# Kernel tuning notes

Hardware: AMD Instinct MI355X
Metric: run time of the kernel (lower is better)

Reference implementation:

```python
import jax, jax.numpy as jnp
import numpy as np

RADIUS = 0.5
BATCH, N, C_IN, C_OUT = 8, 1024, 64, 64


def setup_inputs() -> dict:
    key = jax.random.key(0)
    k1, k2, k3 = jax.random.split(key, 3)
    features = jax.random.normal(k1, (BATCH, N, C_IN), dtype=jnp.float32)
    geometry = jax.random.normal(k2, (BATCH, N, 3), dtype=jnp.float32)
    # Kernel stand-in: linear map from relative position to [C_out, C_in] matrix
    W = jax.random.normal(k3, (3, C_OUT, C_IN), dtype=jnp.float32) / np.sqrt(3.0 * C_IN)
    return {"features": features, "geometry": geometry, "W": W}


def reference(features, geometry, W):
    # diff[z,a,b,:] = r_b - r_a  (neighbor minus center), matching rb - ra in torch
    diff = geometry[:, None, :, :] - geometry[:, :, None, :]          # [z,a,b,3]
    norm = jnp.sqrt(jnp.sum(diff * diff, axis=-1))                    # [z,a,b]
    # rel_mask: 1 where within radius (the dense equivalent of the padded
    # neighbor-list + mask; padded/out-of-ball entries contribute zero)
    rel_mask = (norm < RADIUS).astype(features.dtype)                 # [z,a,b]
    # kernel(diff)[z,a,b,i,j] = sum_x diff[z,a,b,x] * W[x,i,j]
    # output[z,a,i] = sum_{b,x,j} mask*diff[z,a,b,x] * W[x,i,j] * feat[z,b,j]
    mdiff = rel_mask[..., None] * diff                                # [z,a,b,3]
    tmp = jnp.einsum('zabx,zbj->zaxj', mdiff, features)               # [z,a,3,Cin]
    out = jnp.einsum('zaxj,xij->zai', tmp, W)                         # [z,a,Cout]
    return out
```

## Files before the change

### kernel.cpp

```cpp
#include <hip/hip_runtime.h>


#define BATCHSZ 8
#define NPTS 1024
#define CIN 64
#define COUT 64
#define NXJ (3 * CIN)
#define NG (NXJ / 4)
#define PPB 8
#define BS (PPB * 64)
#define CAP 128
#define GPW (NG / PPB)

#define SM_LR 3072
#define SM_TMP 7168
#define SM_TOTAL 8704

__global__ __launch_bounds__(256) void transpose_W_kernel(
    const float* __restrict__ W,
    float* __restrict__ Wt)
{
    const int t = blockIdx.x * 256 + threadIdx.x;
    if (t >= 3 * COUT * CIN) return;
    const int x = t >> 12;
    const int i = (t >> 6) & 63;
    const int j = t & 63;
    const int xj = x * CIN + j;
    Wt[((xj >> 2) * COUT + i) * 4 + (xj & 3)] = W[t];
}

template <bool WT>
__global__ __launch_bounds__(BS, 8) void neigh_conv_kernel(
    const float* __restrict__ feat,
    const float* __restrict__ geom,
    const float* __restrict__ Wv,
    float* __restrict__ out)
{
    const int lane = threadIdx.x & 63;
    const int wv   = threadIdx.x >> 6;
    const int p    = blockIdx.x * PPB + wv;
    const int a    = p & (NPTS - 1);
    const int z    = p >> 10;

    __shared__ __align__(16) float smem[SM_TOTAL];

    {
        const float4* src = (const float4*)(geom + (size_t)z * NPTS * 3);
        float4* dst = (float4*)smem;
        for (int k = threadIdx.x; k < NPTS * 3 / 4; k += BS)
            dst[k] = src[k];
    }
    __syncthreads();

    const float* geo = smem;
    const float gax = geo[a * 3 + 0];
    const float gay = geo[a * 3 + 1];
    const float gaz = geo[a * 3 + 2];
    const float* fz = feat + (size_t)z * NPTS * CIN;

    int*   lb = (int*)(smem + SM_LR) + wv * 512;
    float* lx = smem + SM_LR + wv * 512 + 128;
    float* ly = lx + 128;
    float* lz = ly + 128;

    const unsigned long long ltmask = (1ull << lane) - 1ull;
    float acc0 = 0.f, acc1 = 0.f, acc2 = 0.f;
    int nn = 0;

    #pragma unroll 4
    for (int bb = 0; bb < NPTS; bb += 64) {
        const int b = bb + lane;
        float dx, dy, dz, d2;
        {
            #pragma clang fp contract(off)
            dx = geo[b * 3 + 0] - gax;
            dy = geo[b * 3 + 1] - gay;
            dz = geo[b * 3 + 2] - gaz;
            d2 = dx * dx + dy * dy + dz * dz;
        }
        const bool hit = d2 < 0.25f;
        const unsigned long long m = __ballot(hit);
        const int c = __popcll(m);
        if (nn + c <= CAP) {
            if (hit) {
                const int s = nn + __popcll(m & ltmask);
                lb[s] = b; lx[s] = dx; ly[s] = dy; lz[s] = dz;
            }
            nn += c;
        } else {
            unsigned long long mm = m;
            while (mm) {
                const int src = __ffsll(mm) - 1;
                mm &= mm - 1ull;
                const float ddx = __shfl(dx, src);
                const float ddy = __shfl(dy, src);
                const float ddz = __shfl(dz, src);
                const float f = fz[(size_t)(bb + src) * CIN + lane];
                acc0 = fmaf(ddx, f, acc0);
                acc1 = fmaf(ddy, f, acc1);
                acc2 = fmaf(ddz, f, acc2);
            }
        }
    }

    {
        const int npad = (4 - (nn & 3)) & 3;
        if (lane < npad) {
            lb[nn + lane] = a;
            lx[nn + lane] = 0.f; ly[nn + lane] = 0.f; lz[nn + lane] = 0.f;
        }
        nn += npad;
    }

    for (int k = 0; k < nn; k += 4) {
        const int b0 = lb[k + 0], b1 = lb[k + 1], b2 = lb[k + 2], b3 = lb[k + 3];
        const float f0 = fz[(size_t)b0 * CIN + lane];
        const float f1 = fz[(size_t)b1 * CIN + lane];
        const float f2 = fz[(size_t)b2 * CIN + lane];
        const float f3 = fz[(size_t)b3 * CIN + lane];
        const float x0 = lx[k + 0], y0 = ly[k + 0], z0 = lz[k + 0];
        const float x1 = lx[k + 1], y1 = ly[k + 1], z1 = lz[k + 1];
        const float x2 = lx[k + 2], y2 = ly[k + 2], z2 = lz[k + 2];
        const float x3 = lx[k + 3], y3 = ly[k + 3], z3 = lz[k + 3];
        acc0 = fmaf(x0, f0, acc0); acc1 = fmaf(y0, f0, acc1); acc2 = fmaf(z0, f0, acc2);
        acc0 = fmaf(x1, f1, acc0); acc1 = fmaf(y1, f1, acc1); acc2 = fmaf(z1, f1, acc2);
        acc0 = fmaf(x2, f2, acc0); acc1 = fmaf(y2, f2, acc1); acc2 = fmaf(z2, f2, acc2);
        acc0 = fmaf(x3, f3, acc0); acc1 = fmaf(y3, f3, acc1); acc2 = fmaf(z3, f3, acc2);
    }

    float* tmp = smem + SM_TMP + wv * NXJ;
    tmp[0 * CIN + lane] = acc0;
    tmp[1 * CIN + lane] = acc1;
    tmp[2 * CIN + lane] = acc2;
    __syncthreads();

    const int g0 = wv * GPW;
    float4 wr[GPW];
    if (WT) {
        const float4* w4 = (const float4*)Wv;
        #pragma unroll
        for (int q = 0; q < GPW; ++q)
            wr[q] = w4[(g0 + q) * COUT + lane];
    } else {
        #pragma unroll
        for (int q = 0; q < GPW; ++q) {
            const int xj = 4 * (g0 + q);
            wr[q].x = Wv[((xj + 0) >> 6) * 4096 + lane * 64 + ((xj + 0) & 63)];
            wr[q].y = Wv[((xj + 1) >> 6) * 4096 + lane * 64 + ((xj + 1) & 63)];
            wr[q].z = Wv[((xj + 2) >> 6) * 4096 + lane * 64 + ((xj + 2) & 63)];
            wr[q].w = Wv[((xj + 3) >> 6) * 4096 + lane * 64 + ((xj + 3) & 63)];
        }
    }

    float* red = smem + SM_LR;
    #pragma unroll
    for (int pp = 0; pp < PPB; ++pp) {
        const float4* t4 = (const float4*)(smem + SM_TMP + pp * NXJ);
        float acc = 0.f;
        #pragma unroll
        for (int q = 0; q < GPW; ++q) {
            const float4 t = t4[g0 + q];
            acc = fmaf(t.x, wr[q].x, acc);
            acc = fmaf(t.y, wr[q].y, acc);
            acc = fmaf(t.z, wr[q].z, acc);
            acc = fmaf(t.w, wr[q].w, acc);
        }
        red[(wv * PPB + pp) * COUT + lane] = acc;
    }
    __syncthreads();

    float o = 0.f;
    #pragma unroll
    for (int w = 0; w < PPB; ++w)
        o += red[(w * PPB + wv) * COUT + lane];

    out[(size_t)p * COUT + lane] = o;
}

extern "C" void kernel_launch(void* const* d_in, const int* in_sizes, int n_in,
                              void* d_out, int out_size, void* d_ws, size_t ws_size,
                              hipStream_t stream) {
    const float* feat = (const float*)d_in[0];
    const float* geom = (const float*)d_in[1];
    const float* W    = (const float*)d_in[2];
    float* out        = (float*)d_out;

    const int nblocks = BATCHSZ * NPTS / PPB;

    if (ws_size >= (size_t)(3 * COUT * CIN) * sizeof(float)) {
        float* Wt = (float*)d_ws;
        transpose_W_kernel<<<(3 * COUT * CIN + 255) / 256, 256, 0, stream>>>(W, Wt);
        neigh_conv_kernel<true><<<nblocks, BS, 0, stream>>>(feat, geom, Wt, out);
    } else {
        neigh_conv_kernel<false><<<nblocks, BS, 0, stream>>>(feat, geom, W, out);
    }
}
```

Before: 21.08 us.

## Pack neighbor list as float4, vectorize geometry loads, use packed FMA

Each neighbor entry (dx, dy, dz and the index bit-cast to float) is now stored as one float4, so the gather loop does one wide LDS read per neighbor instead of four scalar ones. The geometry scan reads three float4 per lane covering four points, which changes the order in which neighbors are visited. Accumulation now uses 2-wide float vectors so the compiler can emit packed FMA, and launch_bounds occupancy drops from 8 to 4. The new visit order changes summation order in the overflow path, and the lower occupancy hint may change register allocation.

```diff
diff --git a/kernel.cpp b/kernel.cpp
--- a/kernel.cpp
+++ b/kernel.cpp
@@ -11,6 +11,8 @@
 #define BS (PPB * 64)
 #define CAP 128
 #define GPW (NG / PPB)
+
+typedef float f32x2 __attribute__((ext_vector_type(2)));
 
 #define SM_LR 3072
 #define SM_TMP 7168
@@ -30,7 +32,7 @@
 }
 
 template <bool WT>
-__global__ __launch_bounds__(BS, 8) void neigh_conv_kernel(
+__global__ __launch_bounds__(BS, 4) void neigh_conv_kernel(
     const float* __restrict__ feat,
     const float* __restrict__ geom,
     const float* __restrict__ Wv,
@@ -58,47 +60,58 @@
     const float gaz = geo[a * 3 + 2];
     const float* fz = feat + (size_t)z * NPTS * CIN;
 
-    int*   lb = (int*)(smem + SM_LR) + wv * 512;
-    float* lx = smem + SM_LR + wv * 512 + 128;
-    float* ly = lx + 128;
-    float* lz = ly + 128;
-
+    float4* list4 = (float4*)(smem + SM_LR) + wv * CAP;
     const unsigned long long ltmask = (1ull << lane) - 1ull;
-    float acc0 = 0.f, acc1 = 0.f, acc2 = 0.f;
+
+    f32x2 axy = {0.f, 0.f};
+    float az2 = 0.f;
     int nn = 0;
 
-    #pragma unroll 4
-    for (int bb = 0; bb < NPTS; bb += 64) {
-        const int b = bb + lane;
-        float dx, dy, dz, d2;
-        {
-            #pragma clang fp contract(off)
-            dx = geo[b * 3 + 0] - gax;
-            dy = geo[b * 3 + 1] - gay;
-            dz = geo[b * 3 + 2] - gaz;
-            d2 = dx * dx + dy * dy + dz * dz;
-        }
-        const bool hit = d2 < 0.25f;
-        const unsigned long long m = __ballot(hit);
-        const int c = __popcll(m);
-        if (nn + c <= CAP) {
-            if (hit) {
-                const int s = nn + __popcll(m & ltmask);
-                lb[s] = b; lx[s] = dx; ly[s] = dy; lz[s] = dz;
+    const float4* g4 = (const float4*)geo;
+    for (int ss = 0; ss < 4; ++ss) {
+        const int fbase = ss * 192 + lane * 3;
+        const float4 q0 = g4[fbase + 0];
+        const float4 q1 = g4[fbase + 1];
+        const float4 q2 = g4[fbase + 2];
+        float cx[4] = {q0.x, q0.w, q1.z, q2.y};
+        float cy[4] = {q0.y, q1.x, q1.w, q2.z};
+        float cz[4] = {q0.z, q1.y, q2.x, q2.w};
+        #pragma unroll
+        for (int s = 0; s < 4; ++s) {
+            float dx, dy, dz, d2;
+            {
+                #pragma clang fp contract(off)
+                dx = cx[s] - gax;
+                dy = cy[s] - gay;
+                dz = cz[s] - gaz;
+                d2 = dx * dx + dy * dy + dz * dz;
             }
-            nn += c;
-        } else {
-            unsigned long long mm = m;
-            while (mm) {
-                const int src = __ffsll(mm) - 1;
-                mm &= mm - 1ull;
-                const float ddx = __shfl(dx, src);
-                const float ddy = __shfl(dy, src);
-                const float ddz = __shfl(dz, src);
-                const float f = fz[(size_t)(bb + src) * CIN + lane];
-                acc0 = fmaf(ddx, f, acc0);
-                acc1 = fmaf(ddy, f, acc1);
-                acc2 = fmaf(ddz, f, acc2);
+            const bool hit = d2 < 0.25f;
+            const unsigned long long m = __ballot(hit);
+            const int c = __popcll(m);
+            const int b = ss * 256 + 4 * lane + s;
+            if (nn + c <= CAP) {
+                if (hit) {
+                    const int slot = nn + __popcll(m & ltmask);
+                    float4 e;
+                    e.x = dx; e.y = dy; e.z = dz; e.w = __int_as_float(b);
+                    list4[slot] = e;
+                }
+                nn += c;
+            } else {
+                unsigned long long mm = m;
+                while (mm) {
+                    const int src = __ffsll(mm) - 1;
+                    mm &= mm - 1ull;
+                    const float ddx = __shfl(dx, src);
+                    const float ddy = __shfl(dy, src);
+                    const float ddz = __shfl(dz, src);
+                    const int bsrc = ss * 256 + 4 * src + s;
+                    const float f = fz[(size_t)bsrc * CIN + lane];
+                    axy.x = fmaf(ddx, f, axy.x);
+                    axy.y = fmaf(ddy, f, axy.y);
+                    az2   = fmaf(ddz, f, az2);
+                }
             }
         }
     }
@@ -106,32 +119,37 @@
     {
         const int npad = (4 - (nn & 3)) & 3;
         if (lane < npad) {
-            lb[nn + lane] = a;
-            lx[nn + lane] = 0.f; ly[nn + lane] = 0.f; lz[nn + lane] = 0.f;
+            float4 e;
+            e.x = 0.f; e.y = 0.f; e.z = 0.f; e.w = __int_as_float(a);
+            list4[nn + lane] = e;
         }
         nn += npad;
     }
 
     for (int k = 0; k < nn; k += 4) {
-        const int b0 = lb[k + 0], b1 = lb[k + 1], b2 = lb[k + 2], b3 = lb[k + 3];
-        const float f0 = fz[(size_t)b0 * CIN + lane];
-        const float f1 = fz[(size_t)b1 * CIN + lane];
-        const float f2 = fz[(size_t)b2 * CIN + lane];
-        const float f3 = fz[(size_t)b3 * CIN + lane];
-        const float x0 = lx[k + 0], y0 = ly[k + 0], z0 = lz[k + 0];
-        const float x1 = lx[k + 1], y1 = ly[k + 1], z1 = lz[k + 1];
-        const float x2 = lx[k + 2], y2 = ly[k + 2], z2 = lz[k + 2];
-        const float x3 = lx[k + 3], y3 = ly[k + 3], z3 = lz[k + 3];
-        acc0 = fmaf(x0, f0, acc0); acc1 = fmaf(y0, f0, acc1); acc2 = fmaf(z0, f0, acc2);
-        acc0 = fmaf(x1, f1, acc0); acc1 = fmaf(y1, f1, acc1); acc2 = fmaf(z1, f1, acc2);
-        acc0 = fmaf(x2, f2, acc0); acc1 = fmaf(y2, f2, acc1); acc2 = fmaf(z2, f2, acc2);
-        acc0 = fmaf(x3, f3, acc0); acc1 = fmaf(y3, f3, acc1); acc2 = fmaf(z3, f3, acc2);
+        const float4 e0 = list4[k + 0];
+        const float4 e1 = list4[k + 1];
+        const float4 e2 = list4[k + 2];
+        const float4 e3 = list4[k + 3];
+        const float f0 = fz[(size_t)__float_as_int(e0.w) * CIN + lane];
+        const float f1 = fz[(size_t)__float_as_int(e1.w) * CIN + lane];
+        const float f2 = fz[(size_t)__float_as_int(e2.w) * CIN + lane];
+        const float f3 = fz[(size_t)__float_as_int(e3.w) * CIN + lane];
+        f32x2 d01; d01.x = e0.x; d01.y = e0.y;
+        f32x2 d11; d11.x = e1.x; d11.y = e1.y;
+        f32x2 d21; d21.x = e2.x; d21.y = e2.y;
+        f32x2 d31; d31.x = e3.x; d31.y = e3.y;
+        f32x2 ff0 = {f0, f0}, ff1 = {f1, f1}, ff2 = {f2, f2}, ff3 = {f3, f3};
+        axy = d01 * ff0 + axy;  az2 = fmaf(e0.z, f0, az2);
+        axy = d11 * ff1 + axy;  az2 = fmaf(e1.z, f1, az2);
+        axy = d21 * ff2 + axy;  az2 = fmaf(e2.z, f2, az2);
+        axy = d31 * ff3 + axy;  az2 = fmaf(e3.z, f3, az2);
     }
 
     float* tmp = smem + SM_TMP + wv * NXJ;
-    tmp[0 * CIN + lane] = acc0;
-    tmp[1 * CIN + lane] = acc1;
-    tmp[2 * CIN + lane] = acc2;
+    tmp[0 * CIN + lane] = axy.x;
+    tmp[1 * CIN + lane] = axy.y;
+    tmp[2 * CIN + lane] = az2;
     __syncthreads();
 
     const int g0 = wv * GPW;
@@ -156,16 +174,18 @@
     #pragma unroll
     for (int pp = 0; pp < PPB; ++pp) {
         const float4* t4 = (const float4*)(smem + SM_TMP + pp * NXJ);
-        float acc = 0.f;
+        f32x2 facc = {0.f, 0.f};
         #pragma unroll
         for (int q = 0; q < GPW; ++q) {
             const float4 t = t4[g0 + q];
-            acc = fmaf(t.x, wr[q].x, acc);
-            acc = fmaf(t.y, wr[q].y, acc);
-            acc = fmaf(t.z, wr[q].z, acc);
-            acc = fmaf(t.w, wr[q].w, acc);
-        }
-        red[(wv * PPB + pp) * COUT + lane] = acc;
+            f32x2 ta; ta.x = t.x; ta.y = t.y;
+            f32x2 tb; tb.x = t.z; tb.y = t.w;
+            f32x2 wa; wa.x = wr[q].x; wa.y = wr[q].y;
+            f32x2 wb; wb.x = wr[q].z; wb.y = wr[q].w;
+            facc = ta * wa + facc;
+            facc = tb * wb + facc;
+        }
+        red[(wv * PPB + pp) * COUT + lane] = facc.x + facc.y;
     }
     __syncthreads();
 
```

New measurement: 22.29 us. 1.06x slower.

## Replace LDS neighbor list with per-step ballot masks and packed FMA reduction

Applied to the files above, without the earlier changes.

Drops the shared-memory compacted neighbor list. The kernel now precomputes 16 ballot masks in registers, then iterates set bits directly, recomputing dx/dy/dz from the geometry held in LDS. The W register preload is hoisted before the geometry staging so its latency overlaps the staging, and the W contraction uses 2-wide float vectors so the compiler can emit packed FMA. The change avoids LDS list writes and reads and the overflow path, at the cost of serial per-neighbor feature loads without 4-way batching and extra register pressure from the mask array.

```diff
diff --git a/kernel.cpp b/kernel.cpp
--- a/kernel.cpp
+++ b/kernel.cpp
@@ -9,10 +9,12 @@
 #define NG (NXJ / 4)
 #define PPB 8
 #define BS (PPB * 64)
-#define CAP 128
 #define GPW (NG / PPB)
+#define NSTEP (NPTS / 64)
 
-#define SM_LR 3072
+typedef float f32x2 __attribute__((ext_vector_type(2)));
+
+#define SM_RED 3072
 #define SM_TMP 7168
 #define SM_TOTAL 8704
 
@@ -44,96 +46,6 @@
 
     __shared__ __align__(16) float smem[SM_TOTAL];
 
-    {
-        const float4* src = (const float4*)(geom + (size_t)z * NPTS * 3);
-        float4* dst = (float4*)smem;
-        for (int k = threadIdx.x; k < NPTS * 3 / 4; k += BS)
-            dst[k] = src[k];
-    }
-    __syncthreads();
-
-    const float* geo = smem;
-    const float gax = geo[a * 3 + 0];
-    const float gay = geo[a * 3 + 1];
-    const float gaz = geo[a * 3 + 2];
-    const float* fz = feat + (size_t)z * NPTS * CIN;
-
-    int*   lb = (int*)(smem + SM_LR) + wv * 512;
-    float* lx = smem + SM_LR + wv * 512 + 128;
-    float* ly = lx + 128;
-    float* lz = ly + 128;
-
-    const unsigned long long ltmask = (1ull << lane) - 1ull;
-    float acc0 = 0.f, acc1 = 0.f, acc2 = 0.f;
-    int nn = 0;
-
-    #pragma unroll 4
-    for (int bb = 0; bb < NPTS; bb += 64) {
-        const int b = bb + lane;
-        float dx, dy, dz, d2;
-        {
-            #pragma clang fp contract(off)
-            dx = geo[b * 3 + 0] - gax;
-            dy = geo[b * 3 + 1] - gay;
-            dz = geo[b * 3 + 2] - gaz;
-            d2 = dx * dx + dy * dy + dz * dz;
-        }
-        const bool hit = d2 < 0.25f;
-        const unsigned long long m = __ballot(hit);
-        const int c = __popcll(m);
-        if (nn + c <= CAP) {
-            if (hit) {
-                const int s = nn + __popcll(m & ltmask);
-                lb[s] = b; lx[s] = dx; ly[s] = dy; lz[s] = dz;
-            }
-            nn += c;
-        } else {
-            unsigned long long mm = m;
-            while (mm) {
-                const int src = __ffsll(mm) - 1;
-                mm &= mm - 1ull;
-                const float ddx = __shfl(dx, src);
-                const float ddy = __shfl(dy, src);
-                const float ddz = __shfl(dz, src);
-                const float f = fz[(size_t)(bb + src) * CIN + lane];
-                acc0 = fmaf(ddx, f, acc0);
-                acc1 = fmaf(ddy, f, acc1);
-                acc2 = fmaf(ddz, f, acc2);
-            }
-        }
-    }
-
-    {
-        const int npad = (4 - (nn & 3)) & 3;
-        if (lane < npad) {
-            lb[nn + lane] = a;
-            lx[nn + lane] = 0.f; ly[nn + lane] = 0.f; lz[nn + lane] = 0.f;
-        }
-        nn += npad;
-    }
-
-    for (int k = 0; k < nn; k += 4) {
-        const int b0 = lb[k + 0], b1 = lb[k + 1], b2 = lb[k + 2], b3 = lb[k + 3];
-        const float f0 = fz[(size_t)b0 * CIN + lane];
-        const float f1 = fz[(size_t)b1 * CIN + lane];
-        const float f2 = fz[(size_t)b2 * CIN + lane];
-        const float f3 = fz[(size_t)b3 * CIN + lane];
-        const float x0 = lx[k + 0], y0 = ly[k + 0], z0 = lz[k + 0];
-        const float x1 = lx[k + 1], y1 = ly[k + 1], z1 = lz[k + 1];
-        const float x2 = lx[k + 2], y2 = ly[k + 2], z2 = lz[k + 2];
-        const float x3 = lx[k + 3], y3 = ly[k + 3], z3 = lz[k + 3];
-        acc0 = fmaf(x0, f0, acc0); acc1 = fmaf(y0, f0, acc1); acc2 = fmaf(z0, f0, acc2);
-        acc0 = fmaf(x1, f1, acc0); acc1 = fmaf(y1, f1, acc1); acc2 = fmaf(z1, f1, acc2);
-        acc0 = fmaf(x2, f2, acc0); acc1 = fmaf(y2, f2, acc1); acc2 = fmaf(z2, f2, acc2);
-        acc0 = fmaf(x3, f3, acc0); acc1 = fmaf(y3, f3, acc1); acc2 = fmaf(z3, f3, acc2);
-    }
-
-    float* tmp = smem + SM_TMP + wv * NXJ;
-    tmp[0 * CIN + lane] = acc0;
-    tmp[1 * CIN + lane] = acc1;
-    tmp[2 * CIN + lane] = acc2;
-    __syncthreads();
-
     const int g0 = wv * GPW;
     float4 wr[GPW];
     if (WT) {
@@ -152,20 +64,78 @@
         }
     }
 
-    float* red = smem + SM_LR;
+    {
+        const float4* src = (const float4*)(geom + (size_t)z * NPTS * 3);
+        float4* dst = (float4*)smem;
+        for (int k = threadIdx.x; k < NPTS * 3 / 4; k += BS)
+            dst[k] = src[k];
+    }
+    __syncthreads();
+
+    const float* geo = smem;
+    const float gax = geo[a * 3 + 0];
+    const float gay = geo[a * 3 + 1];
+    const float gaz = geo[a * 3 + 2];
+    const float* fz = feat + (size_t)z * NPTS * CIN;
+
+    unsigned long long masks[NSTEP];
+    #pragma unroll
+    for (int ss = 0; ss < NSTEP; ++ss) {
+        const int b = ss * 64 + lane;
+        float d2;
+        {
+            #pragma clang fp contract(off)
+            const float dx = geo[b * 3 + 0] - gax;
+            const float dy = geo[b * 3 + 1] - gay;
+            const float dz = geo[b * 3 + 2] - gaz;
+            d2 = dx * dx + dy * dy + dz * dz;
+        }
+        masks[ss] = __ballot(d2 < 0.25f);
+    }
+
+    float acc0 = 0.f, acc1 = 0.f, acc2 = 0.f;
+    #pragma unroll
+    for (int ss = 0; ss < NSTEP; ++ss) {
+        unsigned long long mm = masks[ss];
+        while (mm) {
+            const int src = __ffsll(mm) - 1;
+            mm &= mm - 1ull;
+            const int b = ss * 64 + src;
+            const float gbx = geo[b * 3 + 0];
+            const float gby = geo[b * 3 + 1];
+            const float gbz = geo[b * 3 + 2];
+            const float dx = gbx - gax;
+            const float dy = gby - gay;
+            const float dz = gbz - gaz;
+            const float f = fz[(size_t)b * CIN + lane];
+            acc0 = fmaf(dx, f, acc0);
+            acc1 = fmaf(dy, f, acc1);
+            acc2 = fmaf(dz, f, acc2);
+        }
+    }
+
+    float* tmp = smem + SM_TMP + wv * NXJ;
+    tmp[0 * CIN + lane] = acc0;
+    tmp[1 * CIN + lane] = acc1;
+    tmp[2 * CIN + lane] = acc2;
+    __syncthreads();
+
+    float* red = smem + SM_RED;
     #pragma unroll
     for (int pp = 0; pp < PPB; ++pp) {
         const float4* t4 = (const float4*)(smem + SM_TMP + pp * NXJ);
-        float acc = 0.f;
+        f32x2 facc = {0.f, 0.f};
         #pragma unroll
         for (int q = 0; q < GPW; ++q) {
             const float4 t = t4[g0 + q];
-            acc = fmaf(t.x, wr[q].x, acc);
-            acc = fmaf(t.y, wr[q].y, acc);
-            acc = fmaf(t.z, wr[q].z, acc);
-            acc = fmaf(t.w, wr[q].w, acc);
+            f32x2 ta; ta.x = t.x; ta.y = t.y;
+            f32x2 tb; tb.x = t.z; tb.y = t.w;
+            f32x2 wa; wa.x = wr[q].x; wa.y = wr[q].y;
+            f32x2 wb; wb.x = wr[q].z; wb.y = wr[q].w;
+            facc = ta * wa + facc;
+            facc = tb * wb + facc;
         }
-        red[(wv * PPB + pp) * COUT + lane] = acc;
+        red[(wv * PPB + pp) * COUT + lane] = facc.x + facc.y;
     }
     __syncthreads();
 
```

Result: slower. 22.39 us (median of 2 runs) (+6.2%).
